# Kernel tuning notes

Measured on AMD Instinct MI355X. Metric: run time of the kernel, lower is better.

Reference implementation:

```python
import jax, jax.numpy as jnp
import numpy as np

NH = 12
D = 768
HD = D // NH
F = 3072
EPS = 1e-6
SCALE = 1.0 / np.sqrt(HD).astype(np.float32)


def _ln(x, g, b):
    m = x.mean(-1, keepdims=True)
    v = ((x - m) ** 2).mean(-1, keepdims=True)
    return (x - m) / jnp.sqrt(v + EPS) * g + b


def _heads(t):
    B, S, _ = t.shape
    return t.reshape(B, S, NH, HD).transpose(0, 2, 1, 3)  # [B,H,S,hd]


def _attn(q, k, v):
    # q,k,v: [B,H,S,hd]; dropout rate is 0 so omitted
    s = jnp.einsum('bhqd,bhkd->bhqk', q, k) * SCALE
    p = jax.nn.softmax(s, axis=-1)
    c = jnp.einsum('bhqk,bhkd->bhqd', p, v)
    B, H, S, _ = c.shape
    return c.transpose(0, 2, 1, 3).reshape(B, S, D)


def _mlp(x, W1, b1, W2, b2):
    h = jax.nn.gelu(x @ W1 + b1)  # dropout rate 0.1 -> identity (eval)
    return h @ W2 + b2


def setup_inputs() -> dict:
    key = jax.random.key(0)
    ks = jax.random.split(key, 16)
    B, S = 4, 1024
    rnd = lambda k, sh: (jax.random.normal(k, sh, jnp.float32) * 0.02)
    inp = {
        'x': jax.random.normal(ks[0], (B, S, D), jnp.float32),
        'y': jax.random.normal(ks[1], (B, S, D), jnp.float32),
        'ln1x_g': jnp.ones((D,)), 'ln1x_b': jnp.zeros((D,)),
        'ln1y_g': jnp.ones((D,)), 'ln1y_b': jnp.zeros((D,)),
        'Wq': rnd(ks[2], (D, D)), 'bq': jnp.zeros((D,)),
        'Wk': rnd(ks[3], (D, D)), 'bk': jnp.zeros((D,)),
        'Wv': rnd(ks[4], (D, D)), 'bv': jnp.zeros((D,)),
        'Wo': rnd(ks[5], (D, D)), 'bo': jnp.zeros((D,)),
        'Wqd': rnd(ks[6], (D, D)), 'bqd': jnp.zeros((D,)),
        'Wkd': rnd(ks[7], (D, D)), 'bkd': jnp.zeros((D,)),
        'Wvd': rnd(ks[8], (D, D)), 'bvd': jnp.zeros((D,)),
        'Wod': rnd(ks[9], (D, D)), 'bod': jnp.zeros((D,)),
        'w11': jnp.full((1,), 0.5), 'w12': jnp.full((1,), 0.5),
        'w21': jnp.full((1,), 0.5), 'w22': jnp.full((1,), 0.5),
        'ln2x_g': jnp.ones((D,)), 'ln2x_b': jnp.zeros((D,)),
        'ln2y_g': jnp.ones((D,)), 'ln2y_b': jnp.zeros((D,)),
        'W1': rnd(ks[10], (D, F)), 'b1': jnp.zeros((F,)),
        'W2': rnd(ks[11], (F, D)), 'b2': jnp.zeros((D,)),
        'W1d': rnd(ks[12], (D, F)), 'b1d': jnp.zeros((F,)),
        'W2d': rnd(ks[13], (F, D)), 'b2d': jnp.zeros((D,)),
    }
    return inp


def reference(x, y, ln1x_g, ln1x_b, ln1y_g, ln1y_b,
              Wq, bq, Wk, bk, Wv, bv, Wo, bo,
              Wqd, bqd, Wkd, bkd, Wvd, bvd, Wod, bod,
              w11, w12, w21, w22,
              ln2x_g, ln2x_b, ln2y_g, ln2y_b,
              W1, b1, W2, b2, W1d, b1d, W2d, b2d):
    hx, hy = x, y
    xn = _ln(x, ln1x_g, ln1x_b)
    yn = _ln(y, ln1y_g, ln1y_b)
    q = _heads(xn @ Wq + bq); k = _heads(xn @ Wk + bk); v = _heads(xn @ Wv + bv)
    qd = _heads(yn @ Wqd + bqd); kd = _heads(yn @ Wkd + bkd); vd = _heads(yn @ Wvd + bvd)
    a_sx = _attn(q, k, v) @ Wo + bo          # self-x
    a_sy = _attn(qd, kd, vd) @ Wod + bod     # self-y
    a_cx = _attn(q, kd, vd) @ Wo + bo        # cross x-query into y
    a_cy = _attn(qd, k, v) @ Wod + bod       # cross y-query into x
    ax = w11 * a_sx + w12 * a_cx
    ay = w21 * a_sy + w22 * a_cy
    x = ax + hx
    y = ay + hy
    hx, hy = x, y
    x = _mlp(_ln(x, ln2x_g, ln2x_b), W1, b1, W2, b2) + hx
    y = _mlp(_ln(y, ln2y_g, ln2y_b), W1d, b1d, W2d, b2d) + hy
    return (x, y)
```

## Files before the change

kernel.cpp:

```cpp
#include <hip/hip_runtime.h>

typedef unsigned short u16;
typedef unsigned short u16x8 __attribute__((ext_vector_type(8)));
typedef short s16x8 __attribute__((ext_vector_type(8)));
typedef float f32x4 __attribute__((ext_vector_type(4)));

#define EL ((size_t)3145728)
#define DDE ((size_t)589824)
#define DFE ((size_t)2359296)

#if __has_builtin(__builtin_amdgcn_exp2f)
#define EXP2(x) __builtin_amdgcn_exp2f(x)
#else
#define EXP2(x) __expf((x) * 0.6931471805599453f)
#endif

__device__ __forceinline__ float b2f(u16 u) {
    return __builtin_bit_cast(float, (unsigned)u << 16);
}
__device__ __forceinline__ u16 f2bf(float f) {
    unsigned x = __builtin_bit_cast(unsigned, f);
    return (u16)((x + 0x7fffu + ((x >> 16) & 1u)) >> 16);
}
__device__ __forceinline__ float gelu_f(float x) {
    float t = x + 0.044715f * x * x * x;
    return x * __builtin_amdgcn_rcpf(1.0f + EXP2(-2.302207417f * t));
}
__device__ __forceinline__ f32x4 mfma16(s16x8 a, s16x8 b, f32x4 c) {
    return __builtin_amdgcn_mfma_f32_16x16x32_bf16(a, b, c, 0, 0, 0);
}
__device__ __forceinline__ void gld16(const u16* g, u16* l) {
    __builtin_amdgcn_global_load_lds((const __attribute__((address_space(1))) void*)g,
                                     (__attribute__((address_space(3))) void*)l,
                                     16, 0, 0);
}

__global__ __launch_bounds__(256) void transpose8_k(const float* p0, const float* p1,
                                                    const float* p2, const float* p3,
                                                    const float* p4, const float* p5,
                                                    const float* p6, const float* p7,
                                                    u16* __restrict__ dst0) {
    int z = blockIdx.z;
    const float* in = z == 0 ? p0 : z == 1 ? p1 : z == 2 ? p2 : z == 3 ? p3
                    : z == 4 ? p4 : z == 5 ? p5 : z == 6 ? p6 : p7;
    u16* out = dst0 + (size_t)z * DDE;
    const int K = 768, N = 768;
    __shared__ u16 tile[64][72];
    int k0 = blockIdx.y << 6, n0 = blockIdx.x << 6;
    int tid = threadIdx.x;
    int r = tid >> 2, c = (tid & 3) << 4;
    const float* ip = in + (size_t)(k0 + r) * N + n0 + c;
#pragma unroll
    for (int q = 0; q < 4; ++q) {
        f32x4 v = *(const f32x4*)(ip + 4 * q);
#pragma unroll
        for (int e = 0; e < 4; ++e) tile[r][c + 4 * q + e] = f2bf(v[e]);
    }
    __syncthreads();
    u16x8 o0, o1;
#pragma unroll
    for (int e = 0; e < 8; ++e) { o0[e] = tile[c + e][r]; o1[e] = tile[c + 8 + e][r]; }
    u16* op = out + (size_t)(n0 + r) * K + k0 + c;
    *(u16x8*)op = o0;
    *(u16x8*)(op + 8) = o1;
}

__global__ __launch_bounds__(256) void transpose2_k(const float* pa, const float* pb,
                                                    u16* __restrict__ dst0, size_t dsz,
                                                    int K, int N) {
    int z = blockIdx.z;
    const float* in = z ? pb : pa;
    u16* out = dst0 + (size_t)z * dsz;
    __shared__ u16 tile[64][72];
    int k0 = blockIdx.y << 6, n0 = blockIdx.x << 6;
    int tid = threadIdx.x;
    int r = tid >> 2, c = (tid & 3) << 4;
    const float* ip = in + (size_t)(k0 + r) * N + n0 + c;
#pragma unroll
    for (int q = 0; q < 4; ++q) {
        f32x4 v = *(const f32x4*)(ip + 4 * q);
#pragma unroll
        for (int e = 0; e < 4; ++e) tile[r][c + 4 * q + e] = f2bf(v[e]);
    }
    __syncthreads();
    u16x8 o0, o1;
#pragma unroll
    for (int e = 0; e < 8; ++e) { o0[e] = tile[c + e][r]; o1[e] = tile[c + 8 + e][r]; }
    u16* op = out + (size_t)(n0 + r) * K + k0 + c;
    *(u16x8*)op = o0;
    *(u16x8*)(op + 8) = o1;
}

__global__ __launch_bounds__(256) void ln_k(const float* __restrict__ inX,
                                            const float* __restrict__ inY,
                                            const float* gX, const float* bX,
                                            const float* gY, const float* bY,
                                            u16* __restrict__ out0) {
    int z = blockIdx.y;
    const float* in = z ? inY : inX;
    const float* g = z ? gY : gX;
    const float* be = z ? bY : bX;
    u16* out = out0 + (size_t)z * EL;
    int row = blockIdx.x, tid = threadIdx.x;
    const float* p = in + (size_t)row * 768;
    float v0 = p[tid], v1 = p[tid + 256], v2 = p[tid + 512];
    float s = v0 + v1 + v2;
    float q = v0 * v0 + v1 * v1 + v2 * v2;
#pragma unroll
    for (int m = 1; m < 64; m <<= 1) { s += __shfl_xor(s, m); q += __shfl_xor(q, m); }
    __shared__ float red[8];
    int w = tid >> 6, lane = tid & 63;
    if (lane == 0) { red[w] = s; red[4 + w] = q; }
    __syncthreads();
    s = red[0] + red[1] + red[2] + red[3];
    q = red[4] + red[5] + red[6] + red[7];
    float mean = s * (1.0f / 768.0f);
    float var = q * (1.0f / 768.0f) - mean * mean;
    float rstd = rsqrtf(var + 1e-6f);
    u16* o = out + (size_t)row * 768;
    o[tid]       = f2bf((v0 - mean) * rstd * g[tid]       + be[tid]);
    o[tid + 256] = f2bf((v1 - mean) * rstd * g[tid + 256] + be[tid + 256]);
    o[tid + 512] = f2bf((v2 - mean) * rstd * g[tid + 512] + be[tid + 512]);
}

__global__ __launch_bounds__(256) void blend_k(u16* __restrict__ a0,
                                               const u16* __restrict__ b0,
                                               const float* w11, const float* w12,
                                               const float* w21, const float* w22,
                                               int n8) {
    int z = blockIdx.z;
    u16* a = a0 + (size_t)z * EL;
    const u16* b = b0 + (size_t)z * EL;
    float wa = z ? *w21 : *w11, wb = z ? *w22 : *w12;
    for (int i = blockIdx.x * blockDim.x + threadIdx.x; i < n8;
         i += gridDim.x * blockDim.x) {
        u16x8 va = ((const u16x8*)a)[i];
        u16x8 vb = ((const u16x8*)b)[i];
        u16x8 r;
#pragma unroll
        for (int e = 0; e < 8; ++e) r[e] = f2bf(wa * b2f(va[e]) + wb * b2f(vb[e]));
        ((u16x8*)a)[i] = r;
    }
}

#define EPI_PLAIN 0
#define EPI_GELU 3

template <int EPI>
__global__ __launch_bounds__(256) void gemm_k(
    const u16* __restrict__ A0, size_t Asz,
    const u16* __restrict__ B0, size_t Bsz,
    const float* __restrict__ bias0, const float* __restrict__ bias1,
    void* __restrict__ C0, size_t Csz,
    int M, int N, int K) {
    int z = blockIdx.z;
    const u16* A = A0 + z * Asz;
    const u16* BT = B0 + z * Bsz;
    const float* bias = z ? bias1 : bias0;
    u16* Cb = (u16*)C0 + z * Csz;
    float* Cf = (float*)C0 + z * Csz;
    __shared__ u16 lA[2][4096];
    __shared__ u16 lB[2][4096];
    int tid = threadIdx.x;
    int bm0 = blockIdx.y << 7, bn0 = blockIdx.x << 7;
    int lane = tid & 63, wid = tid >> 6;
    int fr = lane & 15, g = lane >> 4;
    int wm = wid >> 1, wn = wid & 1;
    const u16* srcA0 = A + (size_t)(bm0 + (tid & 127)) * K + ((tid >> 7) << 3);
    const u16* srcA1 = srcA0 + 16;
    const u16* srcB0 = BT + (size_t)(bn0 + (tid & 127)) * K + ((tid >> 7) << 3);
    const u16* srcB1 = srcB0 + 16;
    auto STAGE = [&](int buf, int k0) {
        gld16(srcA0 + k0, &lA[buf][0] + tid * 8);
        gld16(srcA1 + k0, &lA[buf][0] + 2048 + tid * 8);
        gld16(srcB0 + k0, &lB[buf][0] + tid * 8);
        gld16(srcB1 + k0, &lB[buf][0] + 2048 + tid * 8);
    };
    f32x4 acc[4][4] = {};
    STAGE(0, 0);
    __syncthreads();
    int cur = 0;
    for (int k0 = 0; k0 < K; k0 += 32) {
        if (k0 + 32 < K) STAGE(cur ^ 1, k0 + 32);
        s16x8 af[4], bf[4];
#pragma unroll
        for (int i = 0; i < 4; ++i)
            af[i] = *(const s16x8*)&lA[cur][(g * 128 + wm * 64 + i * 16 + fr) * 8];
#pragma unroll
        for (int j = 0; j < 4; ++j)
            bf[j] = *(const s16x8*)&lB[cur][(g * 128 + wn * 64 + j * 16 + fr) * 8];
#pragma unroll
        for (int i = 0; i < 4; ++i)
#pragma unroll
            for (int j = 0; j < 4; ++j)
                acc[i][j] = mfma16(af[i], bf[j], acc[i][j]);
        __syncthreads();
        cur ^= 1;
    }
#pragma unroll
    for (int j = 0; j < 4; ++j) {
        int n = bn0 + wn * 64 + j * 16 + fr;
        float bv = bias ? bias[n] : 0.0f;
#pragma unroll
        for (int i = 0; i < 4; ++i) {
#pragma unroll
            for (int r = 0; r < 4; ++r) {
                int m = bm0 + wm * 64 + i * 16 + (g << 2) + r;
                float v = acc[i][j][r] + bv;
                if (EPI == EPI_GELU) Cb[(size_t)m * N + n] = f2bf(gelu_f(v));
                else                 Cf[(size_t)m * N + n] = v;
            }
        }
    }
}

template <int EPI>
__global__ __launch_bounds__(256) void gemm64_k(
    const u16* __restrict__ A0, size_t Asz,
    const u16* __restrict__ B0, size_t Bsz,
    const float* __restrict__ bias0, const float* __restrict__ bias1,
    const float* __restrict__ r0, const float* __restrict__ r1,
    const float* s1a, const float* s1b, const float* s2a, const float* s2b,
    void* __restrict__ C0, size_t Csz,
    int M, int N, int K) {
    int z = blockIdx.z;
    const u16* A = A0 + z * Asz;
    const u16* BT = B0 + z * Bsz;
    const float* bias = z ? bias1 : bias0;
    const float* resid = z ? r1 : r0;
    float* Cf = (float*)C0 + z * Csz;
    u16* Cb = (u16*)C0 + z * Csz;
    __shared__ u16 lA[2][8192];
    __shared__ u16 lB[2][4096];
    int tid = threadIdx.x, lane = tid & 63, wid = tid >> 6;
    int bm0 = blockIdx.y << 7, bn0 = blockIdx.x << 6;
    int fr = lane & 15, g = lane >> 4;
    const u16* sAg = A + (size_t)(bm0 + (tid & 127)) * K + ((tid >> 7) << 3);
    const u16* sBg = BT + (size_t)(bn0 + (tid & 63)) * K + ((tid >> 6) << 3);
    auto STAGE = [&](int buf, int k0) {
#pragma unroll
        for (int q = 0; q < 4; ++q)
            gld16(sAg + k0 + q * 16, &lA[buf][q * 2048 + tid * 8]);
#pragma unroll
        for (int q = 0; q < 2; ++q)
            gld16(sBg + k0 + q * 32, &lB[buf][q * 2048 + tid * 8]);
    };
    f32x4 acc[2][4] = {};
    STAGE(0, 0);
    __syncthreads();
    int cur = 0;
    for (int k0 = 0; k0 < K; k0 += 64) {
        if (k0 + 64 < K) STAGE(cur ^ 1, k0 + 64);
#pragma unroll
        for (int ks = 0; ks < 2; ++ks) {
            s16x8 af[2], bf[4];
#pragma unroll
            for (int i = 0; i < 2; ++i)
                af[i] = *(const s16x8*)&lA[cur][((ks * 4 + g) * 128 + wid * 32 + i * 16 + fr) * 8];
#pragma unroll
            for (int j = 0; j < 4; ++j)
                bf[j] = *(const s16x8*)&lB[cur][((ks * 4 + g) * 64 + j * 16 + fr) * 8];
#pragma unroll
            for (int i = 0; i < 2; ++i)
#pragma unroll
                for (int j = 0; j < 4; ++j)
                    acc[i][j] = mfma16(af[i], bf[j], acc[i][j]);
        }
        __syncthreads();
        cur ^= 1;
    }
    float bscale = 1.0f;
    if (s1a) bscale = z ? (s2a[0] + s2b[0]) : (s1a[0] + s1b[0]);
#pragma unroll
    for (int j = 0; j < 4; ++j) {
        int n = bn0 + j * 16 + fr;
        float bv = bias ? bias[n] * bscale : 0.0f;
#pragma unroll
        for (int i = 0; i < 2; ++i) {
#pragma unroll
            for (int r = 0; r < 4; ++r) {
                int m = bm0 + wid * 32 + i * 16 + (g << 2) + r;
                float v = acc[i][j][r] + bv;
                if (EPI == EPI_PLAIN) {
                    if (resid) v += resid[(size_t)m * N + n];
                    Cf[(size_t)m * N + n] = v;
                } else {
                    Cb[(size_t)m * N + n] = f2bf(gelu_f(v));
                }
            }
        }
    }
}

__global__ __launch_bounds__(256) void gemm_qkv_k(const u16* __restrict__ A0,
                                                  const u16* __restrict__ B0,
                                                  const float* bq, const float* bk,
                                                  const float* bv, const float* bqd,
                                                  const float* bkd, const float* bvd,
                                                  u16* __restrict__ Qd,
                                                  u16* __restrict__ Kd,
                                                  u16* __restrict__ Vd) {
    const int K = 768;
    int z = blockIdx.z;
    const u16* A = A0 + z * EL;
    const u16* BT = B0 + z * 3 * DDE;
    __shared__ u16 lA[2][4096];
    __shared__ u16 lB[2][4096];
    int tid = threadIdx.x;
    int bm0 = blockIdx.y << 7, bn0 = blockIdx.x << 7;
    int lane = tid & 63, wid = tid >> 6, wm = wid >> 1, wn = wid & 1;
    int fr = lane & 15, g = lane >> 4;
    const u16* srcA0 = A + (size_t)(bm0 + (tid & 127)) * K + ((tid >> 7) << 3);
    const u16* srcA1 = srcA0 + 16;
    const u16* srcB0 = BT + (size_t)(bn0 + (tid & 127)) * K + ((tid >> 7) << 3);
    const u16* srcB1 = srcB0 + 16;
    auto STAGE = [&](int buf, int k0) {
        gld16(srcA0 + k0, &lA[buf][0] + tid * 8);
        gld16(srcA1 + k0, &lA[buf][0] + 2048 + tid * 8);
        gld16(srcB0 + k0, &lB[buf][0] + tid * 8);
        gld16(srcB1 + k0, &lB[buf][0] + 2048 + tid * 8);
    };
    f32x4 acc[4][4] = {};
    STAGE(0, 0);
    __syncthreads();
    int cur = 0;
    for (int k0 = 0; k0 < K; k0 += 32) {
        if (k0 + 32 < K) STAGE(cur ^ 1, k0 + 32);
        s16x8 af[4], bf[4];
#pragma unroll
        for (int i = 0; i < 4; ++i)
            af[i] = *(const s16x8*)&lA[cur][(g * 128 + wm * 64 + i * 16 + fr) * 8];
#pragma unroll
        for (int j = 0; j < 4; ++j)
            bf[j] = *(const s16x8*)&lB[cur][(g * 128 + wn * 64 + j * 16 + fr) * 8];
#pragma unroll
        for (int i = 0; i < 4; ++i)
#pragma unroll
            for (int j = 0; j < 4; ++j)
                acc[i][j] = mfma16(af[i], bf[j], acc[i][j]);
        __syncthreads();
        cur ^= 1;
    }
    int seg = bn0 / 768;
    const float* bp = seg == 0 ? (z ? bqd : bq) : seg == 1 ? (z ? bkd : bk) : (z ? bvd : bv);
    u16* out = (seg == 0 ? Qd : seg == 1 ? Kd : Vd) + (size_t)z * 3 * EL;
    int nbase = bn0 - seg * 768;
    const float qs = 0.180336880f;
#pragma unroll
    for (int j = 0; j < 4; ++j) {
        int nn = nbase + wn * 64 + j * 16 + fr;
        float bvl = bp[nn];
        int hh = nn >> 6, hd = nn & 63;
#pragma unroll
        for (int i = 0; i < 4; ++i) {
#pragma unroll
            for (int r = 0; r < 4; ++r) {
                int m = bm0 + wm * 64 + i * 16 + (g << 2) + r;
                int bb = m >> 10, ss = m & 1023;
                size_t o = ((size_t)(bb * 12 + hh)) << 16;
                if (seg < 2) o += ((size_t)ss << 6) + hd;
                else         o += ((size_t)hd << 10) + ss;
                float v = acc[i][j][r] + bvl;
                if (seg == 0) v *= qs;
                out[o] = f2bf(v);
            }
        }
    }
}

__global__ __launch_bounds__(256) void attn_k(const u16* __restrict__ Qx,
                                              const u16* __restrict__ Kx,
                                              const u16* __restrict__ VTx,
                                              const u16* __restrict__ Qy,
                                              const u16* __restrict__ Ky,
                                              const u16* __restrict__ VTy,
                                              u16* __restrict__ csx,
                                              u16* __restrict__ ccx,
                                              u16* __restrict__ csy,
                                              u16* __restrict__ ccy) {
    int p = blockIdx.x;
    int lg = (p & 7) * 192 + (p >> 3);
    int sg = lg >> 4, wi = lg & 15;
    int qt = wi & 7, sub = wi >> 3;
    int pairi = sg / 48, bh = sg % 48;
    int cfg = pairi == 0 ? (sub ? 3 : 0) : (sub ? 2 : 1);
    const u16 *Qp, *Kp, *Vp;
    u16* Op;
    if (cfg == 0)      { Qp = Qx; Kp = Kx; Vp = VTx; Op = csx; }
    else if (cfg == 1) { Qp = Qy; Kp = Ky; Vp = VTy; Op = csy; }
    else if (cfg == 2) { Qp = Qx; Kp = Ky; Vp = VTy; Op = ccx; }
    else               { Qp = Qy; Kp = Kx; Vp = VTx; Op = ccy; }
    const u16* Qh = Qp + ((size_t)bh << 16);
    const u16* Kh = Kp + ((size_t)bh << 16);
    const u16* Vh = Vp + ((size_t)bh << 16);
    int b = bh / 12, h = bh % 12;
    int tid = threadIdx.x, lane = tid & 63, w = tid >> 6;
    int q0 = qt * 128 + w * 32;
    int fr = lane & 15, ko = (lane >> 4) << 3, g = lane >> 4;
    bool glo = lane < 32;
    int srcA = fr + ((lane & 16) << 1);
    int srcB = srcA + 16;

    __shared__ u16 kls[2048];
    __shared__ u16 vls[2048];

    s16x8 qf[2][2];
#pragma unroll
    for (int s = 0; s < 2; ++s) {
        const u16* qp = Qh + (size_t)(q0 + s * 16 + fr) * 64 + ko;
        qf[s][0] = *(const s16x8*)qp;
        qf[s][1] = *(const s16x8*)(qp + 32);
    }

    f32x4 acc[2][4] = {};
    float lsum[2] = {0.f, 0.f};
    f32x4 zz = {0.f, 0.f, 0.f, 0.f};

    int krow = tid >> 3, kpc = tid & 7;
    int kgc = kpc ^ (krow & 7);
    int vdr = tid >> 2, vpv = tid & 3;
    int cK0 = ((fr << 3) + (g ^ (fr & 7))) << 3;
    int cK1 = ((fr << 3) + ((g + 4) ^ (fr & 7))) << 3;
    int cK2 = (((fr + 16) << 3) + (g ^ (fr & 7))) << 3;
    int cK3 = (((fr + 16) << 3) + ((g + 4) ^ (fr & 7))) << 3;

    for (int kb = 0; kb < 1024; kb += 32) {
        gld16(Kh + (size_t)(kb + krow) * 64 + kgc * 8, &kls[tid * 8]);
        gld16(Vh + (size_t)vdr * 1024 + kb + vpv * 8, &vls[tid * 8]);
        __syncthreads();
        s16x8 Kf0 = *(const s16x8*)&kls[cK0];
        s16x8 Kf1 = *(const s16x8*)&kls[cK1];
        s16x8 Kf2 = *(const s16x8*)&kls[cK2];
        s16x8 Kf3 = *(const s16x8*)&kls[cK3];
        s16x8 Vf[4];
#pragma unroll
        for (int t4 = 0; t4 < 4; ++t4)
            Vf[t4] = *(const s16x8*)&vls[((t4 * 16 + fr) << 5) + (g << 3)];
        s16x8 pa[2];
#pragma unroll
        for (int s = 0; s < 2; ++s) {
            __builtin_amdgcn_s_setprio(1);
            f32x4 t0 = mfma16(Kf0, qf[s][0], zz);
            t0 = mfma16(Kf1, qf[s][1], t0);
            f32x4 t1 = mfma16(Kf2, qf[s][0], zz);
            t1 = mfma16(Kf3, qf[s][1], t1);
            __builtin_amdgcn_s_setprio(0);
            float p00 = EXP2(t0[0]), p01 = EXP2(t0[1]);
            float p02 = EXP2(t0[2]), p03 = EXP2(t0[3]);
            float p10 = EXP2(t1[0]), p11 = EXP2(t1[1]);
            float p12 = EXP2(t1[2]), p13 = EXP2(t1[3]);
            lsum[s] += (p00 + p01 + p02 + p03) + (p10 + p11 + p12 + p13);
            unsigned w0, w1, w2, w3;
            asm("v_cvt_pk_bf16_f32 %0, %1, %2" : "=v"(w0) : "v"(p00), "v"(p01));
            asm("v_cvt_pk_bf16_f32 %0, %1, %2" : "=v"(w1) : "v"(p02), "v"(p03));
            asm("v_cvt_pk_bf16_f32 %0, %1, %2" : "=v"(w2) : "v"(p10), "v"(p11));
            asm("v_cvt_pk_bf16_f32 %0, %1, %2" : "=v"(w3) : "v"(p12), "v"(p13));
            int e0 = __shfl((int)w0, srcA), e1 = __shfl((int)w1, srcA);
            int e2 = __shfl((int)w0, srcB), e3 = __shfl((int)w1, srcB);
            int f0 = __shfl((int)w2, srcA), f1 = __shfl((int)w3, srcA);
            int f2 = __shfl((int)w2, srcB), f3 = __shfl((int)w3, srcB);
            int4 wd;
            wd.x = glo ? e0 : f0;
            wd.y = glo ? e1 : f1;
            wd.z = glo ? e2 : f2;
            wd.w = glo ? e3 : f3;
            pa[s] = __builtin_bit_cast(s16x8, wd);
        }
        __builtin_amdgcn_s_setprio(1);
#pragma unroll
        for (int t4 = 0; t4 < 4; ++t4) {
            acc[0][t4] = mfma16(pa[0], Vf[t4], acc[0][t4]);
            acc[1][t4] = mfma16(pa[1], Vf[t4], acc[1][t4]);
        }
        __builtin_amdgcn_s_setprio(0);
        __syncthreads();
    }

    float invv[2][4];
#pragma unroll
    for (int s = 0; s < 2; ++s) {
        float l = lsum[s];
        l += __shfl_xor(l, 16);
        l += __shfl_xor(l, 32);
        float inv = 1.0f / l;
#pragma unroll
        for (int r = 0; r < 4; ++r)
            invv[s][r] = __shfl(inv, ((lane >> 4) << 2) + r);
    }
#pragma unroll
    for (int s = 0; s < 2; ++s) {
        u16* ob = Op + (size_t)(b * 1024 + q0 + s * 16 + ((lane >> 4) << 2)) * 768 + h * 64 + fr;
#pragma unroll
        for (int t4 = 0; t4 < 4; ++t4)
#pragma unroll
            for (int r = 0; r < 4; ++r)
                ob[(size_t)r * 768 + t4 * 16] = f2bf(acc[s][t4][r] * invv[s][r]);
    }
}

extern "C" void kernel_launch(void* const* d_in, const int* in_sizes, int n_in,
                              void* d_out, int out_size, void* d_ws, size_t ws_size,
                              hipStream_t stream) {
    (void)in_sizes; (void)n_in; (void)out_size; (void)ws_size;
    const float* X    = (const float*)d_in[0];
    const float* Y    = (const float*)d_in[1];
    const float* l1xg = (const float*)d_in[2];
    const float* l1xb = (const float*)d_in[3];
    const float* l1yg = (const float*)d_in[4];
    const float* l1yb = (const float*)d_in[5];
    const float* Wq   = (const float*)d_in[6];
    const float* bq   = (const float*)d_in[7];
    const float* Wk   = (const float*)d_in[8];
    const float* bk   = (const float*)d_in[9];
    const float* Wv   = (const float*)d_in[10];
    const float* bv   = (const float*)d_in[11];
    const float* Wo   = (const float*)d_in[12];
    const float* bo   = (const float*)d_in[13];
    const float* Wqd  = (const float*)d_in[14];
    const float* bqd  = (const float*)d_in[15];
    const float* Wkd  = (const float*)d_in[16];
    const float* bkd  = (const float*)d_in[17];
    const float* Wvd  = (const float*)d_in[18];
    const float* bvd  = (const float*)d_in[19];
    const float* Wod  = (const float*)d_in[20];
    const float* bod  = (const float*)d_in[21];
    const float* w11  = (const float*)d_in[22];
    const float* w12  = (const float*)d_in[23];
    const float* w21  = (const float*)d_in[24];
    const float* w22  = (const float*)d_in[25];
    const float* l2xg = (const float*)d_in[26];
    const float* l2xb = (const float*)d_in[27];
    const float* l2yg = (const float*)d_in[28];
    const float* l2yb = (const float*)d_in[29];
    const float* W1   = (const float*)d_in[30];
    const float* b1   = (const float*)d_in[31];
    const float* W2   = (const float*)d_in[32];
    const float* b2   = (const float*)d_in[33];
    const float* W1d  = (const float*)d_in[34];
    const float* b1d  = (const float*)d_in[35];
    const float* W2d  = (const float*)d_in[36];
    const float* b2d  = (const float*)d_in[37];

    u16* ws = (u16*)d_ws;
    u16* qkvT = ws;
    u16* WoT  = qkvT + 6 * DDE;
    u16* W1T  = WoT + 2 * DDE;
    u16* W2T  = W1T + 2 * DFE;
    u16* xn   = W2T + 2 * DFE;
    u16* Qx   = xn + 2 * EL;
    u16* cs   = Qx + 6 * EL;
    float* x1 = (float*)(cs + 4 * EL);
    u16* Kx = Qx + EL;
    u16* VTx = Qx + 2 * EL;
    u16* Qy = Qx + 3 * EL;
    u16* Ky = Qx + 4 * EL;
    u16* VTy = Qx + 5 * EL;
    u16* h = Qx;
    float* y1 = x1 + EL;

    float* out_x = (float*)d_out;

    dim3 tb(256);
    transpose8_k<<<dim3(12, 12, 8), tb, 0, stream>>>(Wq, Wk, Wv, Wqd, Wkd, Wvd, Wo, Wod, qkvT);
    transpose2_k<<<dim3(48, 12, 2), tb, 0, stream>>>(W1, W1d, W1T, DFE, 768, 3072);
    transpose2_k<<<dim3(12, 48, 2), tb, 0, stream>>>(W2, W2d, W2T, DFE, 3072, 768);
    ln_k<<<dim3(4096, 2), tb, 0, stream>>>(X, Y, l1xg, l1xb, l1yg, l1yb, xn);
    gemm_qkv_k<<<dim3(18, 32, 2), tb, 0, stream>>>(xn, qkvT, bq, bk, bv, bqd, bkd, bvd,
                                                   Qx, Kx, VTx);
    attn_k<<<4 * 48 * 8, tb, 0, stream>>>(Qx, Kx, VTx, Qy, Ky, VTy,
                                          cs, cs + 2 * EL, cs + EL, cs + 3 * EL);
    int n8 = (int)(EL / 8);
    blend_k<<<dim3(1536, 1, 2), tb, 0, stream>>>(cs, cs + 2 * EL, w11, w12, w21, w22, n8);
    gemm64_k<EPI_PLAIN><<<dim3(12, 32, 2), tb, 0, stream>>>(
        cs, EL, WoT, DDE, bo, bod, X, Y, w11, w12, w21, w22, x1, EL, 4096, 768, 768);
    ln_k<<<dim3(4096, 2), tb, 0, stream>>>(x1, y1, l2xg, l2xb, l2yg, l2yb, xn);
    gemm_k<EPI_GELU><<<dim3(24, 32, 2), tb, 0, stream>>>(
        xn, EL, W1T, DFE, b1, b1d, h, 4 * EL, 4096, 3072, 768);
    gemm64_k<EPI_PLAIN><<<dim3(12, 32, 2), tb, 0, stream>>>(
        h, 4 * EL, W2T, DFE, b2, b2d, x1, y1, nullptr, nullptr, nullptr, nullptr,
        out_x, EL, 4096, 768, 3072);
}
```

Before: 487.3 us.

## Remap GEMM blocks to XCD-local panels and store residual stream in bf16

GEMM launches become 1D grids, and a mapping function assigns each XCD (block index mod 8) a contiguous set of M-panels across all N tiles, so A-row reuse stays in that XCD's L2. The intermediate residual x1/y1 is now written as bf16 instead of fp32, with a new bf16-input layernorm kernel and a bf16 residual read in the final GEMM epilogue, which halves that traffic. This costs residual precision, since the skip connection is rounded to bf16 before the MLP. The mapping assumes grid sizes divisible by 8 and by the number of N tiles.

After: 458.5 us. -5.9%, faster.

```diff
diff --git a/kernel.cpp b/kernel.cpp
--- a/kernel.cpp
+++ b/kernel.cpp
@@ -33,6 +33,16 @@
     __builtin_amdgcn_global_load_lds((const __attribute__((address_space(1))) void*)g,
                                      (__attribute__((address_space(3))) void*)l,
                                      16, 0, 0);
+}
+__device__ __forceinline__ void xcd_map(int NN, int& m, int& n, int& z) {
+    int p = blockIdx.x, T = gridDim.x;
+    int ppx = T >> 3;
+    int xcd = p & 7, l = p >> 3;
+    int panel = l / NN;
+    n = l - panel * NN;
+    int gp = xcd * (ppx / NN) + panel;
+    z = gp >> 5;
+    m = gp & 31;
 }
 
 __global__ __launch_bounds__(256) void transpose8_k(const float* p0, const float* p1,
@@ -123,6 +133,38 @@
     o[tid + 512] = f2bf((v2 - mean) * rstd * g[tid + 512] + be[tid + 512]);
 }
 
+__global__ __launch_bounds__(256) void lnb_k(const u16* __restrict__ inX,
+                                             const u16* __restrict__ inY,
+                                             const float* gX, const float* bX,
+                                             const float* gY, const float* bY,
+                                             u16* __restrict__ out0) {
+    int z = blockIdx.y;
+    const u16* in = z ? inY : inX;
+    const float* g = z ? gY : gX;
+    const float* be = z ? bY : bX;
+    u16* out = out0 + (size_t)z * EL;
+    int row = blockIdx.x, tid = threadIdx.x;
+    const u16* p = in + (size_t)row * 768;
+    float v0 = b2f(p[tid]), v1 = b2f(p[tid + 256]), v2 = b2f(p[tid + 512]);
+    float s = v0 + v1 + v2;
+    float q = v0 * v0 + v1 * v1 + v2 * v2;
+#pragma unroll
+    for (int m = 1; m < 64; m <<= 1) { s += __shfl_xor(s, m); q += __shfl_xor(q, m); }
+    __shared__ float red[8];
+    int w = tid >> 6, lane = tid & 63;
+    if (lane == 0) { red[w] = s; red[4 + w] = q; }
+    __syncthreads();
+    s = red[0] + red[1] + red[2] + red[3];
+    q = red[4] + red[5] + red[6] + red[7];
+    float mean = s * (1.0f / 768.0f);
+    float var = q * (1.0f / 768.0f) - mean * mean;
+    float rstd = rsqrtf(var + 1e-6f);
+    u16* o = out + (size_t)row * 768;
+    o[tid]       = f2bf((v0 - mean) * rstd * g[tid]       + be[tid]);
+    o[tid + 256] = f2bf((v1 - mean) * rstd * g[tid + 256] + be[tid + 256]);
+    o[tid + 512] = f2bf((v2 - mean) * rstd * g[tid + 512] + be[tid + 512]);
+}
+
 __global__ __launch_bounds__(256) void blend_k(u16* __restrict__ a0,
                                                const u16* __restrict__ b0,
                                                const float* w11, const float* w12,
@@ -143,8 +185,9 @@
     }
 }
 
-#define EPI_PLAIN 0
 #define EPI_GELU 3
+#define EPI_WO 4
+#define EPI_MLP2 5
 
 template <int EPI>
 __global__ __launch_bounds__(256) void gemm_k(
@@ -152,8 +195,9 @@
     const u16* __restrict__ B0, size_t Bsz,
     const float* __restrict__ bias0, const float* __restrict__ bias1,
     void* __restrict__ C0, size_t Csz,
-    int M, int N, int K) {
-    int z = blockIdx.z;
+    int M, int N, int K, int NN) {
+    int m_, n_, z;
+    xcd_map(NN, m_, n_, z);
     const u16* A = A0 + z * Asz;
     const u16* BT = B0 + z * Bsz;
     const float* bias = z ? bias1 : bias0;
@@ -162,7 +206,7 @@
     __shared__ u16 lA[2][4096];
     __shared__ u16 lB[2][4096];
     int tid = threadIdx.x;
-    int bm0 = blockIdx.y << 7, bn0 = blockIdx.x << 7;
+    int bm0 = m_ << 7, bn0 = n_ << 7;
     int lane = tid & 63, wid = tid >> 6;
     int fr = lane & 15, g = lane >> 4;
     int wm = wid >> 1, wn = wid & 1;
@@ -219,21 +263,23 @@
     const u16* __restrict__ A0, size_t Asz,
     const u16* __restrict__ B0, size_t Bsz,
     const float* __restrict__ bias0, const float* __restrict__ bias1,
-    const float* __restrict__ r0, const float* __restrict__ r1,
+    const void* __restrict__ r0, const void* __restrict__ r1,
     const float* s1a, const float* s1b, const float* s2a, const float* s2b,
     void* __restrict__ C0, size_t Csz,
-    int M, int N, int K) {
-    int z = blockIdx.z;
+    int M, int N, int K, int NN) {
+    int m_, n_, z;
+    xcd_map(NN, m_, n_, z);
     const u16* A = A0 + z * Asz;
     const u16* BT = B0 + z * Bsz;
     const float* bias = z ? bias1 : bias0;
-    const float* resid = z ? r1 : r0;
+    const float* residf = (const float*)(z ? r1 : r0);
+    const u16* residb = (const u16*)(z ? r1 : r0);
     float* Cf = (float*)C0 + z * Csz;
     u16* Cb = (u16*)C0 + z * Csz;
     __shared__ u16 lA[2][8192];
     __shared__ u16 lB[2][4096];
     int tid = threadIdx.x, lane = tid & 63, wid = tid >> 6;
-    int bm0 = blockIdx.y << 7, bn0 = blockIdx.x << 6;
+    int bm0 = m_ << 7, bn0 = n_ << 6;
     int fr = lane & 15, g = lane >> 4;
     const u16* sAg = A + (size_t)(bm0 + (tid & 127)) * K + ((tid >> 7) << 3);
     const u16* sBg = BT + (size_t)(bn0 + (tid & 63)) * K + ((tid >> 6) << 3);
@@ -270,22 +316,25 @@
         cur ^= 1;
     }
     float bscale = 1.0f;
-    if (s1a) bscale = z ? (s2a[0] + s2b[0]) : (s1a[0] + s1b[0]);
+    if (EPI == EPI_WO) bscale = z ? (s2a[0] + s2b[0]) : (s1a[0] + s1b[0]);
 #pragma unroll
     for (int j = 0; j < 4; ++j) {
         int n = bn0 + j * 16 + fr;
-        float bv = bias ? bias[n] * bscale : 0.0f;
+        float bv = (z ? bias1 : bias0)[n] * bscale;
+        (void)bias;
 #pragma unroll
         for (int i = 0; i < 2; ++i) {
 #pragma unroll
             for (int r = 0; r < 4; ++r) {
                 int m = bm0 + wid * 32 + i * 16 + (g << 2) + r;
+                size_t idx = (size_t)m * N + n;
                 float v = acc[i][j][r] + bv;
-                if (EPI == EPI_PLAIN) {
-                    if (resid) v += resid[(size_t)m * N + n];
-                    Cf[(size_t)m * N + n] = v;
+                if (EPI == EPI_WO) {
+                    v += residf[idx];
+                    Cb[idx] = f2bf(v);
                 } else {
-                    Cb[(size_t)m * N + n] = f2bf(gelu_f(v));
+                    v += b2f(residb[idx]);
+                    Cf[idx] = v;
                 }
             }
         }
@@ -301,13 +350,14 @@
                                                   u16* __restrict__ Kd,
                                                   u16* __restrict__ Vd) {
     const int K = 768;
-    int z = blockIdx.z;
+    int m_, n_, z;
+    xcd_map(18, m_, n_, z);
     const u16* A = A0 + z * EL;
     const u16* BT = B0 + z * 3 * DDE;
     __shared__ u16 lA[2][4096];
     __shared__ u16 lB[2][4096];
     int tid = threadIdx.x;
-    int bm0 = blockIdx.y << 7, bn0 = blockIdx.x << 7;
+    int bm0 = m_ << 7, bn0 = n_ << 7;
     int lane = tid & 63, wid = tid >> 6, wm = wid >> 1, wn = wid & 1;
     int fr = lane & 15, g = lane >> 4;
     const u16* srcA0 = A + (size_t)(bm0 + (tid & 127)) * K + ((tid >> 7) << 3);
@@ -549,14 +599,14 @@
     u16* xn   = W2T + 2 * DFE;
     u16* Qx   = xn + 2 * EL;
     u16* cs   = Qx + 6 * EL;
-    float* x1 = (float*)(cs + 4 * EL);
+    u16* x1   = cs + 4 * EL;
     u16* Kx = Qx + EL;
     u16* VTx = Qx + 2 * EL;
     u16* Qy = Qx + 3 * EL;
     u16* Ky = Qx + 4 * EL;
     u16* VTy = Qx + 5 * EL;
     u16* h = Qx;
-    float* y1 = x1 + EL;
+    u16* y1 = x1 + EL;
 
     float* out_x = (float*)d_out;
 
@@ -565,18 +615,19 @@
     transpose2_k<<<dim3(48, 12, 2), tb, 0, stream>>>(W1, W1d, W1T, DFE, 768, 3072);
     transpose2_k<<<dim3(12, 48, 2), tb, 0, stream>>>(W2, W2d, W2T, DFE, 3072, 768);
     ln_k<<<dim3(4096, 2), tb, 0, stream>>>(X, Y, l1xg, l1xb, l1yg, l1yb, xn);
-    gemm_qkv_k<<<dim3(18, 32, 2), tb, 0, stream>>>(xn, qkvT, bq, bk, bv, bqd, bkd, bvd,
-                                                   Qx, Kx, VTx);
+    gemm_qkv_k<<<1152, tb, 0, stream>>>(xn, qkvT, bq, bk, bv, bqd, bkd, bvd,
+                                        Qx, Kx, VTx);
     attn_k<<<4 * 48 * 8, tb, 0, stream>>>(Qx, Kx, VTx, Qy, Ky, VTy,
                                           cs, cs + 2 * EL, cs + EL, cs + 3 * EL);
     int n8 = (int)(EL / 8);
     blend_k<<<dim3(1536, 1, 2), tb, 0, stream>>>(cs, cs + 2 * EL, w11, w12, w21, w22, n8);
-    gemm64_k<EPI_PLAIN><<<dim3(12, 32, 2), tb, 0, stream>>>(
-        cs, EL, WoT, DDE, bo, bod, X, Y, w11, w12, w21, w22, x1, EL, 4096, 768, 768);
-    ln_k<<<dim3(4096, 2), tb, 0, stream>>>(x1, y1, l2xg, l2xb, l2yg, l2yb, xn);
-    gemm_k<EPI_GELU><<<dim3(24, 32, 2), tb, 0, stream>>>(
-        xn, EL, W1T, DFE, b1, b1d, h, 4 * EL, 4096, 3072, 768);
-    gemm64_k<EPI_PLAIN><<<dim3(12, 32, 2), tb, 0, stream>>>(
+    gemm64_k<EPI_WO><<<768, tb, 0, stream>>>(
+        cs, EL, WoT, DDE, bo, bod, X, Y, w11, w12, w21, w22, x1, EL,
+        4096, 768, 768, 12);
+    lnb_k<<<dim3(4096, 2), tb, 0, stream>>>(x1, y1, l2xg, l2xb, l2yg, l2yb, xn);
+    gemm_k<EPI_GELU><<<1536, tb, 0, stream>>>(
+        xn, EL, W1T, DFE, b1, b1d, h, 4 * EL, 4096, 3072, 768, 24);
+    gemm64_k<EPI_MLP2><<<768, tb, 0, stream>>>(
         h, 4 * EL, W2T, DFE, b2, b2d, x1, y1, nullptr, nullptr, nullptr, nullptr,
-        out_x, EL, 4096, 768, 3072);
-}
+        out_x, EL, 4096, 768, 3072, 12);
+}
```
